# Kernel optimization log

Hardware: AMD Instinct MI355X
Metric: run time of the kernel (lower is better)

## Reference

```python
import jax, jax.numpy as jnp
import numpy as np

N, E, F, H = 50000, 800000, 256, 64


def setup_inputs() -> dict:
    key = jax.random.key(0)
    ks = jax.random.split(key, 6)
    x = jax.random.normal(ks[0], (N, F), jnp.float32)
    edge_index = jax.random.randint(ks[1], (2, E), 0, N)
    init = lambda k, shp, fan: jax.random.normal(k, shp, jnp.float32) / np.float32(np.sqrt(fan))
    W1l = init(ks[2], (F, H), F)
    b1l = jnp.zeros((H,), jnp.float32)
    W1r = init(ks[3], (F, H), F)
    W2l = init(ks[4], (H, H), H)
    b2l = jnp.zeros((H,), jnp.float32)
    W2r = init(ks[5], (H, H), H)
    return dict(x=x, edge_index=edge_index, W1l=W1l, b1l=b1l, W1r=W1r,
                W2l=W2l, b2l=b2l, W2r=W2r)


def _sage(x, src, dst, Wl, bl, Wr, n):
    # SAGEConv: out = mean_{j->i}(lin_l(x)_j) + lin_r(x)_i
    m = x @ Wl + bl                                   # [N, H]
    agg = jax.ops.segment_sum(m[src], dst, num_segments=n)
    deg = jax.ops.segment_sum(jnp.ones((src.shape[0],), x.dtype), dst, num_segments=n)
    agg = agg / jnp.maximum(deg, 1.0)[:, None]        # mean aggregation
    return agg + x @ Wr


def reference(x, edge_index, W1l, b1l, W1r, W2l, b2l, W2r):
    src, dst = edge_index[0], edge_index[1]
    n = x.shape[0]
    # 2-layer SAGE encoder (dropout=0, no residual for 2 layers)
    h = jax.nn.relu(_sage(x, src, dst, W1l, b1l, W1r, n))
    z = _sage(h, src, dst, W2l, b2l, W2r, n)
    # UnitNorm: replace all-zero rows with randn, then row-wise L2 normalize
    valid = jnp.sum(z != 0, axis=1, keepdims=True) > 0
    r = jax.random.normal(jax.random.key(42), z.shape, z.dtype)
    z = jnp.where(valid, z, r)
    z = z / jnp.sqrt(jnp.sum(z * z, axis=1, keepdims=True))
    # dot-product decode on observed edges + positive-edge BCE loss
    scores = jnp.sum(z[src] * z[dst], axis=-1)        # [E]
    loss = -jnp.mean(jax.nn.log_sigmoid(scores))
    return z, loss
```

## Files before the change

kernel.cpp:

```cpp
#include <hip/hip_runtime.h>

#define N_NODES 50000
#define N_EDGES 800000
#define F_IN    256
#define H_DIM   64
#define NB_SCAN 196
#define TILE_A  4096
#define EPT     (TILE_A / 256)
#define NT_A    ((N_EDGES + TILE_A - 1) / TILE_A)
#define CAP     64
#define MAXB    4544
#define GT1     ((N_NODES + 63) / 64)
#define SUBN    64
#define DEC_GRID ((N_NODES + SUBN - 1) / SUBN)

typedef __attribute__((ext_vector_type(8))) short short8;
typedef __attribute__((ext_vector_type(4))) float floatx4;
typedef __attribute__((ext_vector_type(2))) float floatx2;

__device__ __forceinline__ unsigned short f2bf(float f) {
  unsigned int u;
  __builtin_memcpy(&u, &f, 4);
  u += 0x7fffu + ((u >> 16) & 1u);
  return (unsigned short)(u >> 16);
}
__device__ __forceinline__ float bflo(unsigned int u) {
  unsigned int v = u << 16; float f; __builtin_memcpy(&f, &v, 4); return f;
}
__device__ __forceinline__ float bfhi(unsigned int u) {
  unsigned int v = u & 0xffff0000u; float f; __builtin_memcpy(&f, &v, 4); return f;
}

__device__ __forceinline__ float dot4_fp8(unsigned int a, unsigned int b, float acc) {
  floatx2 a01 = __builtin_amdgcn_cvt_pk_f32_fp8(a, false);
  floatx2 a23 = __builtin_amdgcn_cvt_pk_f32_fp8(a, true);
  floatx2 b01 = __builtin_amdgcn_cvt_pk_f32_fp8(b, false);
  floatx2 b23 = __builtin_amdgcn_cvt_pk_f32_fp8(b, true);
  acc = fmaf(a01[0], b01[0], acc);
  acc = fmaf(a01[1], b01[1], acc);
  acc = fmaf(a23[0], b23[0], acc);
  acc = fmaf(a23[1], b23[1], acc);
  return acc;
}

template<int K>
__device__ __forceinline__ void pack_body(int t, const float* __restrict__ Wl,
                                          const float* __restrict__ Wr,
                                          unsigned short* __restrict__ Wb)
{
  int lane = t & 63;
  int f    = t >> 6;
  int m    = f & 1;
  int c    = (f >> 1) & 3;
  int ks   = f >> 3;
  const float* W = m ? Wr : Wl;
  int quad = lane >> 4, l15 = lane & 15;
  int col = c * 16 + l15;
  unsigned short u[8];
#pragma unroll
  for (int j = 0; j < 8; ++j) {
    int k = ks * 32 + quad * 8 + j;
    u[j] = f2bf(W[k * H_DIM + col]);
  }
  uint4 v;
  __builtin_memcpy(&v, u, 16);
  ((uint4*)Wb)[t] = v;
}

__device__ __forceinline__ void binA2_body(int blk, unsigned char* smem,
                                           const int* __restrict__ ei,
                                           int2* __restrict__ cnt2,
                                           unsigned int* __restrict__ ebuf2)
{
  int* lcnt   = (int*)smem;
  int* lofs   = lcnt + 256;
  int* lstart = lofs + 256;
  int* lcur   = lstart + 256;
  unsigned int* ldata = (unsigned int*)(lcur + 256);
  const int t = threadIdx.x;
  const int e0 = blk * TILE_A;
  lcnt[t] = 0;
  __syncthreads();
  int ss[EPT], ds[EPT];
#pragma unroll
  for (int j = 0; j < EPT; ++j) {
    int e = e0 + t + j * 256;
    if (e < N_EDGES) {
      ss[j] = ei[e];
      ds[j] = ei[N_EDGES + e];
      atomicAdd(&lcnt[ds[j] >> 8], 1);
    } else {
      ds[j] = -1;
    }
  }
  __syncthreads();
  int v = lcnt[t];
  lofs[t] = v;
  __syncthreads();
  for (int off = 1; off < 256; off <<= 1) {
    int u = (t >= off) ? lofs[t - off] : 0;
    __syncthreads();
    lofs[t] += u;
    __syncthreads();
  }
  lstart[t] = lofs[t] - v;
  lcur[t]   = lofs[t] - v;
  __syncthreads();
#pragma unroll
  for (int j = 0; j < EPT; ++j) {
    if (ds[j] >= 0) {
      int p = atomicAdd(&lcur[ds[j] >> 8], 1);
      ldata[p] = ((unsigned int)ss[j] << 8) | (unsigned int)(ds[j] & 255);
    }
  }
  __syncthreads();
  int w = t >> 6, lane = t & 63;
  for (int b = w; b < NB_SCAN; b += 4) {
    int len = min(lcnt[b], CAP);
    int st = lstart[b];
    if (lane == 0) cnt2[blk * NB_SCAN + b] = make_int2(len, st);
    unsigned int* dst = ebuf2 + ((size_t)blk * NB_SCAN + b) * CAP;
    if (lane < len) dst[lane] = ldata[st + lane];
  }
}

__global__ __launch_bounds__(256) void packbinA_k(
    const float* __restrict__ W1l, const float* __restrict__ W1r,
    const float* __restrict__ W2l, const float* __restrict__ W2r,
    unsigned short* __restrict__ Wb1, unsigned short* __restrict__ Wb2,
    float* __restrict__ loss_slot, const int* __restrict__ ei,
    int2* __restrict__ cnt2, unsigned int* __restrict__ ebuf2)
{
  __shared__ __align__(16) unsigned char smem[4 * 1024 + TILE_A * 4];
  int b = blockIdx.x;
  if (b < 16) {
    if (b == 0 && threadIdx.x == 0) loss_slot[0] = 0.f;
    pack_body<F_IN>(b * 256 + threadIdx.x, W1l, W1r, Wb1);
  } else if (b < 20) {
    pack_body<H_DIM>((b - 16) * 256 + threadIdx.x, W2l, W2r, Wb2);
  } else {
    binA2_body(b - 20, smem, ei, cnt2, ebuf2);
  }
}

__device__ __forceinline__ void gemm1_body(
    int bx, unsigned short* xs,
    const float* __restrict__ X_,
    const unsigned short* __restrict__ Wb,
    const float* __restrict__ bl,
    unsigned short* __restrict__ outl, unsigned short* __restrict__ outr)
{
  constexpr int K = F_IN, KP = K + 8;
  const int row0 = bx * 64;
  const float4* X = (const float4*)X_;
  const int CH = K / 4;
  for (int i = threadIdx.x; i < 64 * CH; i += 256) {
    int r = i / CH, c = i % CH;
    int row = row0 + r;
    float4 v = (row < N_NODES) ? X[(size_t)row * CH + c]
                               : make_float4(0.f, 0.f, 0.f, 0.f);
    unsigned int lo = (unsigned int)f2bf(v.x) | ((unsigned int)f2bf(v.y) << 16);
    unsigned int hi = (unsigned int)f2bf(v.z) | ((unsigned int)f2bf(v.w) << 16);
    *(uint2*)&xs[r * KP + c * 4] = make_uint2(lo, hi);
  }
  __syncthreads();

  const int lane = threadIdx.x & 63;
  const int w    = threadIdx.x >> 6;
  const int quad = lane >> 4;
  const int l15  = lane & 15;
  const int rloc = w * 16 + l15;

  floatx4 accl[4], accr[4];
#pragma unroll
  for (int c = 0; c < 4; ++c) { accl[c] = (floatx4)0.f; accr[c] = (floatx4)0.f; }

  const uint4* wbase = (const uint4*)Wb;
#pragma unroll
  for (int ks = 0; ks < K / 32; ++ks) {
    short8 af = *(const short8*)&xs[rloc * KP + ks * 32 + quad * 8];
#pragma unroll
    for (int c = 0; c < 4; ++c) {
      uint4 rl = wbase[((ks * 4 + c) * 2 + 0) * 64 + lane];
      uint4 rr = wbase[((ks * 4 + c) * 2 + 1) * 64 + lane];
      short8 bfl, bfr;
      __builtin_memcpy(&bfl, &rl, 16);
      __builtin_memcpy(&bfr, &rr, 16);
      accl[c] = __builtin_amdgcn_mfma_f32_16x16x32_bf16(af, bfl, accl[c], 0, 0, 0);
      accr[c] = __builtin_amdgcn_mfma_f32_16x16x32_bf16(af, bfr, accr[c], 0, 0, 0);
    }
  }
#pragma unroll
  for (int c = 0; c < 4; ++c) {
    int col = c * 16 + l15;
    float bias = bl[col];
#pragma unroll
    for (int reg = 0; reg < 4; ++reg) {
      int row = row0 + w * 16 + quad * 4 + reg;
      if (row < N_NODES) {
        outl[(size_t)row * H_DIM + col] = f2bf(accl[c][reg] + bias);
        outr[(size_t)row * H_DIM + col] = f2bf(accr[c][reg]);
      }
    }
  }
}

__device__ __forceinline__ void binB3_body(int b, unsigned char* smem,
    const int2* __restrict__ cnt2, const unsigned int* __restrict__ ebuf2,
    int* __restrict__ esrc, int* __restrict__ rowptr)
{
  int* sA    = (int*)smem;
  int* sB    = sA + 256;
  int* ncnt  = sB + 256;
  int* ncur  = ncnt + 256;
  int* sh_se = ncur + 256;
  unsigned int* sdata = (unsigned int*)(sh_se + 4);
  unsigned int* ssrc  = sdata + MAXB;
  const int t = threadIdx.x;

  int cl = 0, ps = 0;
  if (t < NT_A) {
    int2 v = cnt2[t * NB_SCAN + b];
    cl = min(v.x, CAP);
    ps = v.y;
  }
  sA[t] = cl;
  sB[t] = ps;
  __syncthreads();
  for (int off = 128; off > 0; off >>= 1) {
    if (t < off) sB[t] += sB[t + off];
    __syncthreads();
  }
  for (int off = 1; off < 256; off <<= 1) {
    int u = (t >= off) ? sA[t - off] : 0;
    __syncthreads();
    sA[t] += u;
    __syncthreads();
  }
  if (t == 0) { sh_se[0] = sB[0]; sh_se[1] = min(sA[255], MAXB); }
  __syncthreads();
  const int start = sh_se[0], len = sh_se[1];

  int hw = t >> 5, lane32 = t & 31;
  for (int blk = hw; blk < NT_A; blk += 8) {
    int incl = sA[blk];
    int l = incl - (blk ? sA[blk - 1] : 0);
    int o = incl - l;
    const unsigned int* seg = ebuf2 + ((size_t)blk * NB_SCAN + b) * CAP;
    for (int j = lane32; j < l; j += 32)
      if (o + j < MAXB) sdata[o + j] = seg[j];
  }
  __syncthreads();
  ncnt[t] = 0;
  __syncthreads();
  for (int i = t; i < len; i += 256) atomicAdd(&ncnt[sdata[i] & 255], 1);
  __syncthreads();
  int v = ncnt[t];
  for (int off = 1; off < 256; off <<= 1) {
    int u = (t >= off) ? ncnt[t - off] : 0;
    __syncthreads();
    ncnt[t] += u;
    __syncthreads();
  }
  ncur[t] = ncnt[t] - v;
  __syncthreads();
  for (int i = t; i < len; i += 256) {
    unsigned int e = sdata[i];
    int p = atomicAdd(&ncur[e & 255], 1);
    ssrc[p] = e >> 8;
  }
  __syncthreads();
  for (int i = t; i < len; i += 256) esrc[start + i] = (int)ssrc[i];
  int node = b * 256 + t;
  int s0 = start + ncnt[t] - v;
  if (node < N_NODES) {
    rowptr[node] = s0;
    if (node == N_NODES - 1) rowptr[N_NODES] = s0 + v;
  }
}

__global__ __launch_bounds__(256, 4) void binB_gemm1_k(
    const float* __restrict__ x, const unsigned short* __restrict__ Wb1,
    const float* __restrict__ b1l,
    unsigned short* __restrict__ m1, unsigned short* __restrict__ xr,
    const int2* __restrict__ cnt2, const unsigned int* __restrict__ ebuf2,
    int* __restrict__ esrc, int* __restrict__ rowptr)
{
  __shared__ __align__(16) unsigned char smem[4 * 1024 + 16 + 2 * MAXB * 4];
  if (blockIdx.x < GT1) gemm1_body(blockIdx.x, (unsigned short*)smem, x, Wb1, b1l, m1, xr);
  else                  binB3_body(blockIdx.x - GT1, smem, cnt2, ebuf2, esrc, rowptr);
}

__device__ __forceinline__ void agg_quad(const int* __restrict__ esrc,
                                         const unsigned short* __restrict__ m,
                                         int b, int e, int g, int l15,
                                         float* __restrict__ a)
{
  float p0 = 0.f, p1 = 0.f, p2 = 0.f, p3 = 0.f;
  float q0 = 0.f, q1 = 0.f, q2 = 0.f, q3 = 0.f;
  float r0 = 0.f, r1 = 0.f, r2 = 0.f, r3 = 0.f;
  float s0 = 0.f, s1 = 0.f, s2 = 0.f, s3 = 0.f;
  int i = b + g;
  for (; i + 12 < e; i += 16) {
    int sa = esrc[i], sb = esrc[i + 4], sc = esrc[i + 8], sd = esrc[i + 12];
    uint2 va = *(const uint2*)(m + (size_t)sa * H_DIM + l15 * 4);
    uint2 vb = *(const uint2*)(m + (size_t)sb * H_DIM + l15 * 4);
    uint2 vc = *(const uint2*)(m + (size_t)sc * H_DIM + l15 * 4);
    uint2 vd = *(const uint2*)(m + (size_t)sd * H_DIM + l15 * 4);
    p0 += bflo(va.x); p1 += bfhi(va.x); p2 += bflo(va.y); p3 += bfhi(va.y);
    q0 += bflo(vb.x); q1 += bfhi(vb.x); q2 += bflo(vb.y); q3 += bfhi(vb.y);
    r0 += bflo(vc.x); r1 += bfhi(vc.x); r2 += bflo(vc.y); r3 += bfhi(vc.y);
    s0 += bflo(vd.x); s1 += bfhi(vd.x); s2 += bflo(vd.y); s3 += bfhi(vd.y);
  }
  for (; i < e; i += 4) {
    int sa = esrc[i];
    uint2 va = *(const uint2*)(m + (size_t)sa * H_DIM + l15 * 4);
    p0 += bflo(va.x); p1 += bfhi(va.x); p2 += bflo(va.y); p3 += bfhi(va.y);
  }
  a[0] = (p0 + q0) + (r0 + s0);
  a[1] = (p1 + q1) + (r1 + s1);
  a[2] = (p2 + q2) + (r2 + s2);
  a[3] = (p3 + q3) + (r3 + s3);
#pragma unroll
  for (int j = 0; j < 4; ++j) {
    a[j] += __shfl_xor(a[j], 16, 64);
    a[j] += __shfl_xor(a[j], 32, 64);
  }
}

__global__ __launch_bounds__(256) void agg1_k(
    const int* __restrict__ rowptr, const int* __restrict__ esrc,
    const unsigned short* __restrict__ m, const unsigned short* __restrict__ xr,
    unsigned short* __restrict__ h)
{
  int gid = blockIdx.x * 256 + threadIdx.x;
  int row = gid >> 6;
  if (row >= N_NODES) return;
  int lane = threadIdx.x & 63, g = lane >> 4, l15 = lane & 15;
  int b = rowptr[row], e = rowptr[row + 1];
  float a[4];
  agg_quad(esrc, m, b, e, g, l15, a);
  if (g == 0) {
    float inv = 1.f / fmaxf((float)(e - b), 1.f);
    uint2 rx = *(const uint2*)(xr + (size_t)row * H_DIM + l15 * 4);
    float h0 = fmaxf(a[0] * inv + bflo(rx.x), 0.f);
    float h1 = fmaxf(a[1] * inv + bfhi(rx.x), 0.f);
    float h2 = fmaxf(a[2] * inv + bflo(rx.y), 0.f);
    float h3 = fmaxf(a[3] * inv + bfhi(rx.y), 0.f);
    uint2 o;
    o.x = (unsigned int)f2bf(h0) | ((unsigned int)f2bf(h1) << 16);
    o.y = (unsigned int)f2bf(h2) | ((unsigned int)f2bf(h3) << 16);
    *(uint2*)(h + (size_t)row * H_DIM + l15 * 4) = o;
  }
}

__global__ __launch_bounds__(256) void agg2m_k(
    const int* __restrict__ rowptr, const int* __restrict__ esrc,
    const unsigned short* __restrict__ h, unsigned short* __restrict__ aggh)
{
  int gid = blockIdx.x * 256 + threadIdx.x;
  int row = gid >> 6;
  if (row >= N_NODES) return;
  int lane = threadIdx.x & 63, g = lane >> 4, l15 = lane & 15;
  int b = rowptr[row], e = rowptr[row + 1];
  float a[4];
  agg_quad(esrc, h, b, e, g, l15, a);
  if (g == 0) {
    float inv = 1.f / fmaxf((float)(e - b), 1.f);
    uint2 o;
    o.x = (unsigned int)f2bf(a[0] * inv) | ((unsigned int)f2bf(a[1] * inv) << 16);
    o.y = (unsigned int)f2bf(a[2] * inv) | ((unsigned int)f2bf(a[3] * inv) << 16);
    *(uint2*)(aggh + (size_t)row * H_DIM + l15 * 4) = o;
  }
}

__global__ __launch_bounds__(256, 4) void gemm2z_k(
    const unsigned short* __restrict__ h, const unsigned short* __restrict__ aggh,
    const unsigned short* __restrict__ Wb, const float* __restrict__ b2l,
    const int* __restrict__ rowptr,
    float* __restrict__ zout, unsigned char* __restrict__ zb8)
{
  constexpr int KP = H_DIM + 8;
  __shared__ __align__(16) unsigned short xh[64 * KP];
  __shared__ __align__(16) unsigned short xa[64 * KP];
  __shared__ __align__(16) unsigned int z8[64 * 16];
  const int t = threadIdx.x;
  const int row0 = blockIdx.x * 64;
  const uint4* H4 = (const uint4*)h;
  const uint4* A4 = (const uint4*)aggh;
  for (int i = t; i < 64 * 8; i += 256) {
    int r = i >> 3, c = i & 7;
    int row = row0 + r;
    uint4 vh = (row < N_NODES) ? H4[(size_t)row * 8 + c] : make_uint4(0, 0, 0, 0);
    uint4 va = (row < N_NODES) ? A4[(size_t)row * 8 + c] : make_uint4(0, 0, 0, 0);
    *(uint4*)&xh[r * KP + c * 8] = vh;
    *(uint4*)&xa[r * KP + c * 8] = va;
  }
  __syncthreads();

  const int lane = t & 63;
  const int w    = t >> 6;
  const int quad = lane >> 4;
  const int l15  = lane & 15;
  const int rloc = w * 16 + l15;

  floatx4 acc[4];
#pragma unroll
  for (int c = 0; c < 4; ++c) acc[c] = (floatx4)0.f;

  const uint4* wbase = (const uint4*)Wb;
#pragma unroll
  for (int ks = 0; ks < 2; ++ks) {
    short8 ah = *(const short8*)&xh[rloc * KP + ks * 32 + quad * 8];
    short8 aa = *(const short8*)&xa[rloc * KP + ks * 32 + quad * 8];
#pragma unroll
    for (int c = 0; c < 4; ++c) {
      uint4 rl = wbase[((ks * 4 + c) * 2 + 0) * 64 + lane];
      uint4 rr = wbase[((ks * 4 + c) * 2 + 1) * 64 + lane];
      short8 bfl, bfr;
      __builtin_memcpy(&bfl, &rl, 16);
      __builtin_memcpy(&bfr, &rr, 16);
      acc[c] = __builtin_amdgcn_mfma_f32_16x16x32_bf16(aa, bfl, acc[c], 0, 0, 0);
      acc[c] = __builtin_amdgcn_mfma_f32_16x16x32_bf16(ah, bfr, acc[c], 0, 0, 0);
    }
  }

  float bias[4];
#pragma unroll
  for (int c = 0; c < 4; ++c) bias[c] = b2l[c * 16 + l15];
  unsigned char* z8b = (unsigned char*)z8;
#pragma unroll
  for (int reg = 0; reg < 4; ++reg) {
    int rl = w * 16 + quad * 4 + reg;
    int row = row0 + rl;
    float bm = 0.f;
    if (row < N_NODES) bm = (rowptr[row + 1] - rowptr[row]) > 0 ? 1.f : 0.f;
    float v0 = acc[0][reg] + bias[0] * bm;
    float v1 = acc[1][reg] + bias[1] * bm;
    float v2 = acc[2][reg] + bias[2] * bm;
    float v3 = acc[3][reg] + bias[3] * bm;
    float ssum = v0 * v0 + v1 * v1 + v2 * v2 + v3 * v3;
    ssum += __shfl_xor(ssum, 1, 64);
    ssum += __shfl_xor(ssum, 2, 64);
    ssum += __shfl_xor(ssum, 4, 64);
    ssum += __shfl_xor(ssum, 8, 64);
    float rs = rsqrtf(fmaxf(ssum, 1e-30f));
    float z0 = v0 * rs, z1 = v1 * rs, z2 = v2 * rs, z3 = v3 * rs;
    if (row < N_NODES) {
      zout[(size_t)row * H_DIM +  0 + l15] = z0;
      zout[(size_t)row * H_DIM + 16 + l15] = z1;
      zout[(size_t)row * H_DIM + 32 + l15] = z2;
      zout[(size_t)row * H_DIM + 48 + l15] = z3;
    }
    z8b[rl * 64 +  0 + l15] = (unsigned char)(__builtin_amdgcn_cvt_pk_fp8_f32(z0, z0, 0, false) & 0xff);
    z8b[rl * 64 + 16 + l15] = (unsigned char)(__builtin_amdgcn_cvt_pk_fp8_f32(z1, z1, 0, false) & 0xff);
    z8b[rl * 64 + 32 + l15] = (unsigned char)(__builtin_amdgcn_cvt_pk_fp8_f32(z2, z2, 0, false) & 0xff);
    z8b[rl * 64 + 48 + l15] = (unsigned char)(__builtin_amdgcn_cvt_pk_fp8_f32(z3, z3, 0, false) & 0xff);
  }
  __syncthreads();
  int rowt = row0 + (t >> 2);
  if (rowt < N_NODES)
    *(uint4*)(zb8 + (size_t)row0 * 64 + t * 16) = ((const uint4*)z8)[t];
}

__global__ __launch_bounds__(256) void decode_fp8_k(
    const int* __restrict__ rowptr, const int* __restrict__ esrc,
    const unsigned char* __restrict__ zb8, float* __restrict__ loss_slot)
{
  __shared__ __align__(16) unsigned int zrows[SUBN * 16];
  __shared__ int sh_rp[SUBN + 1];
  __shared__ float sbuf[4];
  const int t = threadIdx.x;
  const int node0 = blockIdx.x * SUBN;
  const int nr = min(SUBN, N_NODES - node0);
  for (int i = t; i < nr * 16; i += 256) {
    int r = i >> 4, c = i & 15;
    unsigned int w = ((const unsigned int*)(zb8 + (size_t)(node0 + r) * H_DIM))[c];
    zrows[r * 16 + (c ^ (r & 15))] = w;
  }
  if (t <= nr) sh_rp[t] = rowptr[node0 + t];
  __syncthreads();
  const int estart = sh_rp[0], eend = sh_rp[nr];
  float part = 0.f;
  for (int e = estart + t; e < eend; e += 512) {
    int e2 = e + 256;
    bool has2 = (e2 < eend);
    int lo = 0, hi = nr;
    while (hi - lo > 1) {
      int mid = (lo + hi) >> 1;
      if (sh_rp[mid] <= e) lo = mid; else hi = mid;
    }
    const int r1 = lo;
    hi = nr;
    while (hi - lo > 1) {
      int mid = (lo + hi) >> 1;
      if (sh_rp[mid] <= e2) lo = mid; else hi = mid;
    }
    const int r2 = lo;
    const int s1 = esrc[e];
    const int s2 = has2 ? esrc[e2] : s1;
    const uint4* zs1 = (const uint4*)(zb8 + (size_t)s1 * H_DIM);
    const uint4* zs2 = (const uint4*)(zb8 + (size_t)s2 * H_DIM);
    float p1 = 0.f, p2 = 0.f;
#pragma unroll
    for (int c4 = 0; c4 < 4; ++c4) {
      uint4 a1 = zs1[c4], a2 = zs2[c4];
      unsigned int au1[4] = {a1.x, a1.y, a1.z, a1.w};
      unsigned int au2[4] = {a2.x, a2.y, a2.z, a2.w};
#pragma unroll
      for (int j = 0; j < 4; ++j) {
        int c = c4 * 4 + j;
        unsigned int b1 = zrows[r1 * 16 + (c ^ (r1 & 15))];
        unsigned int b2 = zrows[r2 * 16 + (c ^ (r2 & 15))];
        p1 = dot4_fp8(au1[j], b1, p1);
        p2 = dot4_fp8(au2[j], b2, p2);
      }
    }
    part += fmaxf(-p1, 0.f) + log1pf(expf(-fabsf(p1)));
    if (has2) part += fmaxf(-p2, 0.f) + log1pf(expf(-fabsf(p2)));
  }
#pragma unroll
  for (int m = 32; m >= 1; m >>= 1) part += __shfl_xor(part, m, 64);
  int lane = t & 63, w = t >> 6;
  if (lane == 0) sbuf[w] = part;
  __syncthreads();
  if (t == 0)
    atomicAdd(loss_slot, (sbuf[0] + sbuf[1] + sbuf[2] + sbuf[3]) * (1.0f / N_EDGES));
}

extern "C" void kernel_launch(void* const* d_in, const int* in_sizes, int n_in,
                              void* d_out, int out_size, void* d_ws, size_t ws_size,
                              hipStream_t stream)
{
  (void)in_sizes; (void)n_in; (void)out_size; (void)ws_size;
  const float* x   = (const float*)d_in[0];
  const int*   ei  = (const int*)d_in[1];
  const float* W1l = (const float*)d_in[2];
  const float* b1l = (const float*)d_in[3];
  const float* W1r = (const float*)d_in[4];
  const float* W2l = (const float*)d_in[5];
  const float* b2l = (const float*)d_in[6];
  const float* W2r = (const float*)d_in[7];
  float* out = (float*)d_out;
  float* loss_slot = out + (size_t)N_NODES * H_DIM;

  const size_t NH = (size_t)N_NODES * H_DIM;
  unsigned short* uA = (unsigned short*)d_ws;
  unsigned short* uB = uA + NH;
  unsigned short* uC = uB + NH;
  unsigned short* uD = uC + NH;
  unsigned char*  zb8 = (unsigned char*)uA;
  unsigned short* Wb1 = uD + NH;
  unsigned short* Wb2 = Wb1 + (F_IN / 32) * 4 * 2 * 64 * 8;
  int* rowptr = (int*)(Wb2 + (H_DIM / 32) * 4 * 2 * 64 * 8);
  int* esrc   = rowptr + N_NODES + 1;
  int2* cnt2  = (int2*)(esrc + N_EDGES);
  unsigned int* ebuf2 = (unsigned int*)(cnt2 + NT_A * NB_SCAN);

  dim3 blk(256);
  dim3 g_pa(20 + NT_A);
  dim3 g_fuse(GT1 + NB_SCAN);
  dim3 g_tile(GT1);
  dim3 g_node((N_NODES * 64 + 255) / 256);
  dim3 g_dec(DEC_GRID);

  packbinA_k<<<g_pa, blk, 0, stream>>>(W1l, W1r, W2l, W2r, Wb1, Wb2,
                                       loss_slot, ei, cnt2, ebuf2);
  binB_gemm1_k<<<g_fuse, blk, 0, stream>>>(x, Wb1, b1l, uA, uC,
                                           cnt2, ebuf2, esrc, rowptr);
  agg1_k<<<g_node, blk, 0, stream>>>(rowptr, esrc, uA, uC, uB);
  agg2m_k<<<g_node, blk, 0, stream>>>(rowptr, esrc, uB, uD);
  gemm2z_k<<<g_tile, blk, 0, stream>>>(uB, uD, Wb2, b2l, rowptr, out, zb8);
  decode_fp8_k<<<g_dec, blk, 0, stream>>>(rowptr, esrc, zb8, loss_slot);
}
```

Baseline: 217.1 us.

## Apply layer-2 weights before aggregation and fuse into layer-1 aggregation kernel

Uses linearity of mean aggregation to compute h@W2l and h@W2r per node right after layer-1 aggregation, inside the same kernel via MFMA on a 16-row shared tile. Layer 2 then only aggregates the pre-transformed rows, adds the bias and normalizes, so the separate agg2 and gemm2 kernels and the h/aggh round trips go away. The cost is an extra bf16 rounding point before aggregation, a block-wide sync in 1024-thread blocks, and bias masking that now depends on the degree.

```diff
diff --git a/kernel.cpp b/kernel.cpp
--- a/kernel.cpp
+++ b/kernel.cpp
@@ -13,6 +13,7 @@
 #define GT1     ((N_NODES + 63) / 64)
 #define SUBN    64
 #define DEC_GRID ((N_NODES + SUBN - 1) / SUBN)
+#define AGG_BLOCKS (N_NODES / 16)
 
 typedef __attribute__((ext_vector_type(8))) short short8;
 typedef __attribute__((ext_vector_type(4))) float floatx4;
@@ -328,10 +329,71 @@
   }
 }
 
-__global__ __launch_bounds__(256) void agg1_k(
+__global__ __launch_bounds__(1024) void agg1G_k(
     const int* __restrict__ rowptr, const int* __restrict__ esrc,
-    const unsigned short* __restrict__ m, const unsigned short* __restrict__ xr,
-    unsigned short* __restrict__ h)
+    const unsigned short* __restrict__ m1, const unsigned short* __restrict__ xr,
+    const unsigned short* __restrict__ Wb,
+    unsigned short* __restrict__ G1, unsigned short* __restrict__ G2)
+{
+  constexpr int KP = H_DIM + 8;
+  __shared__ __align__(16) unsigned short hs[16 * KP];
+  const int t = threadIdx.x;
+  const int wv = t >> 6;
+  const int lane = t & 63;
+  const int g = lane >> 4, l15 = lane & 15;
+  const int row0 = blockIdx.x * 16;
+  const int row = row0 + wv;
+
+  {
+    int b = rowptr[row], e = rowptr[row + 1];
+    float a[4];
+    agg_quad(esrc, m1, b, e, g, l15, a);
+    if (g == 0) {
+      float inv = 1.f / fmaxf((float)(e - b), 1.f);
+      uint2 rx = *(const uint2*)(xr + (size_t)row * H_DIM + l15 * 4);
+      float h0 = fmaxf(a[0] * inv + bflo(rx.x), 0.f);
+      float h1 = fmaxf(a[1] * inv + bfhi(rx.x), 0.f);
+      float h2 = fmaxf(a[2] * inv + bflo(rx.y), 0.f);
+      float h3 = fmaxf(a[3] * inv + bfhi(rx.y), 0.f);
+      uint2 o;
+      o.x = (unsigned int)f2bf(h0) | ((unsigned int)f2bf(h1) << 16);
+      o.y = (unsigned int)f2bf(h2) | ((unsigned int)f2bf(h3) << 16);
+      *(uint2*)&hs[wv * KP + l15 * 4] = o;
+    }
+  }
+  __syncthreads();
+
+  if (wv < 4) {
+    const int quad = lane >> 4;
+    floatx4 a1 = (floatx4)0.f, a2 = (floatx4)0.f;
+    const uint4* wbase = (const uint4*)Wb;
+#pragma unroll
+    for (int ks = 0; ks < 2; ++ks) {
+      short8 af = *(const short8*)&hs[l15 * KP + ks * 32 + quad * 8];
+      uint4 rl = wbase[((ks * 4 + wv) * 2 + 0) * 64 + lane];
+      uint4 rr = wbase[((ks * 4 + wv) * 2 + 1) * 64 + lane];
+      short8 bfl, bfr;
+      __builtin_memcpy(&bfl, &rl, 16);
+      __builtin_memcpy(&bfr, &rr, 16);
+      a1 = __builtin_amdgcn_mfma_f32_16x16x32_bf16(af, bfl, a1, 0, 0, 0);
+      a2 = __builtin_amdgcn_mfma_f32_16x16x32_bf16(af, bfr, a2, 0, 0, 0);
+    }
+    int col = wv * 16 + l15;
+#pragma unroll
+    for (int reg = 0; reg < 4; ++reg) {
+      int r = quad * 4 + reg;
+      size_t o = (size_t)(row0 + r) * H_DIM + col;
+      G1[o] = f2bf(a1[reg]);
+      G2[o] = f2bf(a2[reg]);
+    }
+  }
+}
+
+__global__ __launch_bounds__(256) void aggz_k(
+    const int* __restrict__ rowptr, const int* __restrict__ esrc,
+    const unsigned short* __restrict__ G1, const unsigned short* __restrict__ G2,
+    const float* __restrict__ b2l,
+    float* __restrict__ zout, unsigned char* __restrict__ zb8)
 {
   int gid = blockIdx.x * 256 + threadIdx.x;
   int row = gid >> 6;
@@ -339,128 +401,26 @@
   int lane = threadIdx.x & 63, g = lane >> 4, l15 = lane & 15;
   int b = rowptr[row], e = rowptr[row + 1];
   float a[4];
-  agg_quad(esrc, m, b, e, g, l15, a);
+  agg_quad(esrc, G1, b, e, g, l15, a);
+  float inv = 1.f / fmaxf((float)(e - b), 1.f);
+  float bm = (e - b) > 0 ? 1.f : 0.f;
+  uint2 rx = *(const uint2*)(G2 + (size_t)row * H_DIM + l15 * 4);
+  float4 bias = *(const float4*)(b2l + l15 * 4);
+  float v0 = a[0] * inv + bflo(rx.x) + bias.x * bm;
+  float v1 = a[1] * inv + bfhi(rx.x) + bias.y * bm;
+  float v2 = a[2] * inv + bflo(rx.y) + bias.z * bm;
+  float v3 = a[3] * inv + bfhi(rx.y) + bias.w * bm;
+  float ss = v0 * v0 + v1 * v1 + v2 * v2 + v3 * v3;
+#pragma unroll
+  for (int mm = 8; mm >= 1; mm >>= 1) ss += __shfl_xor(ss, mm, 64);
+  float rs = rsqrtf(fmaxf(ss, 1e-30f));
   if (g == 0) {
-    float inv = 1.f / fmaxf((float)(e - b), 1.f);
-    uint2 rx = *(const uint2*)(xr + (size_t)row * H_DIM + l15 * 4);
-    float h0 = fmaxf(a[0] * inv + bflo(rx.x), 0.f);
-    float h1 = fmaxf(a[1] * inv + bfhi(rx.x), 0.f);
-    float h2 = fmaxf(a[2] * inv + bflo(rx.y), 0.f);
-    float h3 = fmaxf(a[3] * inv + bfhi(rx.y), 0.f);
-    uint2 o;
-    o.x = (unsigned int)f2bf(h0) | ((unsigned int)f2bf(h1) << 16);
-    o.y = (unsigned int)f2bf(h2) | ((unsigned int)f2bf(h3) << 16);
-    *(uint2*)(h + (size_t)row * H_DIM + l15 * 4) = o;
-  }
-}
-
-__global__ __launch_bounds__(256) void agg2m_k(
-    const int* __restrict__ rowptr, const int* __restrict__ esrc,
-    const unsigned short* __restrict__ h, unsigned short* __restrict__ aggh)
-{
-  int gid = blockIdx.x * 256 + threadIdx.x;
-  int row = gid >> 6;
-  if (row >= N_NODES) return;
-  int lane = threadIdx.x & 63, g = lane >> 4, l15 = lane & 15;
-  int b = rowptr[row], e = rowptr[row + 1];
-  float a[4];
-  agg_quad(esrc, h, b, e, g, l15, a);
-  if (g == 0) {
-    float inv = 1.f / fmaxf((float)(e - b), 1.f);
-    uint2 o;
-    o.x = (unsigned int)f2bf(a[0] * inv) | ((unsigned int)f2bf(a[1] * inv) << 16);
-    o.y = (unsigned int)f2bf(a[2] * inv) | ((unsigned int)f2bf(a[3] * inv) << 16);
-    *(uint2*)(aggh + (size_t)row * H_DIM + l15 * 4) = o;
-  }
-}
-
-__global__ __launch_bounds__(256, 4) void gemm2z_k(
-    const unsigned short* __restrict__ h, const unsigned short* __restrict__ aggh,
-    const unsigned short* __restrict__ Wb, const float* __restrict__ b2l,
-    const int* __restrict__ rowptr,
-    float* __restrict__ zout, unsigned char* __restrict__ zb8)
-{
-  constexpr int KP = H_DIM + 8;
-  __shared__ __align__(16) unsigned short xh[64 * KP];
-  __shared__ __align__(16) unsigned short xa[64 * KP];
-  __shared__ __align__(16) unsigned int z8[64 * 16];
-  const int t = threadIdx.x;
-  const int row0 = blockIdx.x * 64;
-  const uint4* H4 = (const uint4*)h;
-  const uint4* A4 = (const uint4*)aggh;
-  for (int i = t; i < 64 * 8; i += 256) {
-    int r = i >> 3, c = i & 7;
-    int row = row0 + r;
-    uint4 vh = (row < N_NODES) ? H4[(size_t)row * 8 + c] : make_uint4(0, 0, 0, 0);
-    uint4 va = (row < N_NODES) ? A4[(size_t)row * 8 + c] : make_uint4(0, 0, 0, 0);
-    *(uint4*)&xh[r * KP + c * 8] = vh;
-    *(uint4*)&xa[r * KP + c * 8] = va;
-  }
-  __syncthreads();
-
-  const int lane = t & 63;
-  const int w    = t >> 6;
-  const int quad = lane >> 4;
-  const int l15  = lane & 15;
-  const int rloc = w * 16 + l15;
-
-  floatx4 acc[4];
-#pragma unroll
-  for (int c = 0; c < 4; ++c) acc[c] = (floatx4)0.f;
-
-  const uint4* wbase = (const uint4*)Wb;
-#pragma unroll
-  for (int ks = 0; ks < 2; ++ks) {
-    short8 ah = *(const short8*)&xh[rloc * KP + ks * 32 + quad * 8];
-    short8 aa = *(const short8*)&xa[rloc * KP + ks * 32 + quad * 8];
-#pragma unroll
-    for (int c = 0; c < 4; ++c) {
-      uint4 rl = wbase[((ks * 4 + c) * 2 + 0) * 64 + lane];
-      uint4 rr = wbase[((ks * 4 + c) * 2 + 1) * 64 + lane];
-      short8 bfl, bfr;
-      __builtin_memcpy(&bfl, &rl, 16);
-      __builtin_memcpy(&bfr, &rr, 16);
-      acc[c] = __builtin_amdgcn_mfma_f32_16x16x32_bf16(aa, bfl, acc[c], 0, 0, 0);
-      acc[c] = __builtin_amdgcn_mfma_f32_16x16x32_bf16(ah, bfr, acc[c], 0, 0, 0);
-    }
-  }
-
-  float bias[4];
-#pragma unroll
-  for (int c = 0; c < 4; ++c) bias[c] = b2l[c * 16 + l15];
-  unsigned char* z8b = (unsigned char*)z8;
-#pragma unroll
-  for (int reg = 0; reg < 4; ++reg) {
-    int rl = w * 16 + quad * 4 + reg;
-    int row = row0 + rl;
-    float bm = 0.f;
-    if (row < N_NODES) bm = (rowptr[row + 1] - rowptr[row]) > 0 ? 1.f : 0.f;
-    float v0 = acc[0][reg] + bias[0] * bm;
-    float v1 = acc[1][reg] + bias[1] * bm;
-    float v2 = acc[2][reg] + bias[2] * bm;
-    float v3 = acc[3][reg] + bias[3] * bm;
-    float ssum = v0 * v0 + v1 * v1 + v2 * v2 + v3 * v3;
-    ssum += __shfl_xor(ssum, 1, 64);
-    ssum += __shfl_xor(ssum, 2, 64);
-    ssum += __shfl_xor(ssum, 4, 64);
-    ssum += __shfl_xor(ssum, 8, 64);
-    float rs = rsqrtf(fmaxf(ssum, 1e-30f));
     float z0 = v0 * rs, z1 = v1 * rs, z2 = v2 * rs, z3 = v3 * rs;
-    if (row < N_NODES) {
-      zout[(size_t)row * H_DIM +  0 + l15] = z0;
-      zout[(size_t)row * H_DIM + 16 + l15] = z1;
-      zout[(size_t)row * H_DIM + 32 + l15] = z2;
-      zout[(size_t)row * H_DIM + 48 + l15] = z3;
-    }
-    z8b[rl * 64 +  0 + l15] = (unsigned char)(__builtin_amdgcn_cvt_pk_fp8_f32(z0, z0, 0, false) & 0xff);
-    z8b[rl * 64 + 16 + l15] = (unsigned char)(__builtin_amdgcn_cvt_pk_fp8_f32(z1, z1, 0, false) & 0xff);
-    z8b[rl * 64 + 32 + l15] = (unsigned char)(__builtin_amdgcn_cvt_pk_fp8_f32(z2, z2, 0, false) & 0xff);
-    z8b[rl * 64 + 48 + l15] = (unsigned char)(__builtin_amdgcn_cvt_pk_fp8_f32(z3, z3, 0, false) & 0xff);
-  }
-  __syncthreads();
-  int rowt = row0 + (t >> 2);
-  if (rowt < N_NODES)
-    *(uint4*)(zb8 + (size_t)row0 * 64 + t * 16) = ((const uint4*)z8)[t];
+    *(float4*)(zout + (size_t)row * H_DIM + l15 * 4) = make_float4(z0, z1, z2, z3);
+    unsigned int w8 = (unsigned int)__builtin_amdgcn_cvt_pk_fp8_f32(z0, z1, 0, false);
+    w8 = (unsigned int)__builtin_amdgcn_cvt_pk_fp8_f32(z2, z3, (int)w8, true);
+    ((unsigned int*)(zb8 + (size_t)row * H_DIM))[l15] = w8;
+  }
 }
 
 __global__ __launch_bounds__(256) void decode_fp8_k(
@@ -560,7 +520,7 @@
   dim3 blk(256);
   dim3 g_pa(20 + NT_A);
   dim3 g_fuse(GT1 + NB_SCAN);
-  dim3 g_tile(GT1);
+  dim3 g_ag(AGG_BLOCKS);
   dim3 g_node((N_NODES * 64 + 255) / 256);
   dim3 g_dec(DEC_GRID);
 
@@ -568,8 +528,7 @@
                                        loss_slot, ei, cnt2, ebuf2);
   binB_gemm1_k<<<g_fuse, blk, 0, stream>>>(x, Wb1, b1l, uA, uC,
                                            cnt2, ebuf2, esrc, rowptr);
-  agg1_k<<<g_node, blk, 0, stream>>>(rowptr, esrc, uA, uC, uB);
-  agg2m_k<<<g_node, blk, 0, stream>>>(rowptr, esrc, uB, uD);
-  gemm2z_k<<<g_tile, blk, 0, stream>>>(uB, uD, Wb2, b2l, rowptr, out, zb8);
+  agg1G_k<<<g_ag, dim3(1024), 0, stream>>>(rowptr, esrc, uA, uC, Wb2, uB, uD);
+  aggz_k<<<g_node, blk, 0, stream>>>(rowptr, esrc, uB, uD, b2l, out, zb8);
   decode_fp8_k<<<g_dec, blk, 0, stream>>>(rowptr, esrc, zb8, loss_slot);
 }
```

Result: no change. 219.3 us (+1.0%).
